# Performance work log

Measured on AMD Instinct MI355X. Metric: run time of the kernel, lower is better.

## Reference

```python
import jax, jax.numpy as jnp
import numpy as np

N = 8192
D = 256
LN_EPS = 1e-5
NORM_EPS = 1e-12


def _layernorm(h, gamma, beta):
    mu = jnp.mean(h, axis=-1, keepdims=True)
    var = jnp.var(h, axis=-1, keepdims=True)
    return (h - mu) * jax.lax.rsqrt(var + LN_EPS) * gamma + beta


def _elu(z):
    return jnp.where(z > 0, z, jnp.expm1(z))


def setup_inputs() -> dict:
    key = jax.random.key(0)
    ks = jax.random.split(key, 5)
    s = 1.0 / np.sqrt(D)  # torch Linear default-ish init scale
    h = jax.random.normal(ks[0], (N, D), dtype=jnp.float32)
    x = jax.random.normal(ks[1], (N, D), dtype=jnp.float32)
    Wk = jax.random.normal(ks[2], (D, D), dtype=jnp.float32) * s
    Wq = jax.random.normal(ks[3], (D, D), dtype=jnp.float32) * s
    Wv = jax.random.normal(ks[4], (D, D), dtype=jnp.float32) * s
    ln_gamma = jnp.ones((D,), dtype=jnp.float32)
    ln_beta = jnp.zeros((D,), dtype=jnp.float32)
    semantic_weight = -1.0
    mixing = jnp.array([[semantic_weight, semantic_weight], [0.0, 0.0]], dtype=jnp.float32)
    return {"h": h, "x": x, "Wk": Wk, "Wq": Wq, "Wv": Wv,
            "ln_gamma": ln_gamma, "ln_beta": ln_beta, "mixing": mixing}


def reference(h, x, Wk, Wq, Wv, ln_gamma, ln_beta, mixing):
    h0, x0 = h, x
    hn = _layernorm(h, ln_gamma, ln_beta)                      # [N, D]
    k = hn @ Wk                                                # [N, H]
    q = hn @ Wq                                                # [N, H]
    # semantic attention: softmax over rows of k q^T / sqrt(H)
    a_h = jax.nn.softmax((k @ q.T) * (D ** -0.5), axis=-1)     # [N, N]
    # structural attention: row-L2-normalized gram matrix of x
    g = x @ x.T                                                # [N, N]
    gnorm = jnp.linalg.norm(g, axis=-1, keepdims=True)
    a_x = g / jnp.maximum(gnorm, NORM_EPS)
    # learned 2x2 mixing, softmax over dim 0 (stack @ mixing.softmax(0))
    m = jax.nn.softmax(mixing, axis=0)
    a_h_mix = a_h * m[0, 0] + a_x * m[1, 0]
    a_x_mix = a_h * m[0, 1] + a_x * m[1, 1]
    h_new = _elu((a_h_mix @ hn) @ Wv)                          # [N, D]
    x_new = a_x_mix @ x                                        # [N, D]
    h_new = h_new + h0
    x_new = x_new + x0
    return (h_new, x_new)
```

## Files before the change

kernel.cpp:

```cpp
#include <hip/hip_runtime.h>

#define N 8192
#define D 256

typedef unsigned short u16;
typedef unsigned int u32;
typedef short bf16x8 __attribute__((ext_vector_type(8)));
typedef float f32x4 __attribute__((ext_vector_type(4)));

__device__ __forceinline__ u16 f2bf(float f) {
    u32 u = __float_as_uint(f);
    u += 0x7FFFu + ((u >> 16) & 1u);
    return (u16)(u >> 16);
}
__device__ __forceinline__ float bf2f(u16 v) {
    return __uint_as_float(((u32)v) << 16);
}

#define MFMA(a, b, c) __builtin_amdgcn_mfma_f32_16x16x32_bf16((a), (b), (c), 0, 0, 0)

__global__ __launch_bounds__(256) void k_prep_all(const float* __restrict__ h,
    const float* __restrict__ x, const float* __restrict__ gamma,
    const float* __restrict__ beta, u16* __restrict__ hnb, u16* __restrict__ xb,
    const float* __restrict__ Wk, const float* __restrict__ Wq,
    const float* __restrict__ Wv, u16* __restrict__ wkT,
    u16* __restrict__ wqT, u16* __restrict__ wvT)
{
    int bid = blockIdx.x;
    if (bid < 2048) {
        int lane = threadIdx.x & 63;
        int row = bid * 4 + (threadIdx.x >> 6);
        const float4 hv = ((const float4*)(h + (size_t)row * D))[lane];
        float s = hv.x + hv.y + hv.z + hv.w;
        float s2 = hv.x * hv.x + hv.y * hv.y + hv.z * hv.z + hv.w * hv.w;
#pragma unroll
        for (int m = 1; m < 64; m <<= 1) { s += __shfl_xor(s, m); s2 += __shfl_xor(s2, m); }
        float mu = s * (1.0f / D);
        float var = s2 * (1.0f / D) - mu * mu;
        float rstd = rsqrtf(var + 1e-5f);
        const float4 gv = ((const float4*)gamma)[lane];
        const float4 bv = ((const float4*)beta)[lane];
        ushort4 o;
        o.x = f2bf((hv.x - mu) * rstd * gv.x + bv.x);
        o.y = f2bf((hv.y - mu) * rstd * gv.y + bv.y);
        o.z = f2bf((hv.z - mu) * rstd * gv.z + bv.z);
        o.w = f2bf((hv.w - mu) * rstd * gv.w + bv.w);
        ((ushort4*)(hnb + (size_t)row * D))[lane] = o;
        const float4 xv = ((const float4*)(x + (size_t)row * D))[lane];
        ushort4 xo;
        xo.x = f2bf(xv.x); xo.y = f2bf(xv.y); xo.z = f2bf(xv.z); xo.w = f2bf(xv.w);
        ((ushort4*)(xb + (size_t)row * D))[lane] = xo;
    } else {
        int wid = bid - 2048;
        int sel = wid >> 8;
        int c = wid & 255;
        const float* src = sel == 0 ? Wk : (sel == 1 ? Wq : Wv);
        u16* dst = sel == 0 ? wkT : (sel == 1 ? wqT : wvT);
        int r = threadIdx.x;
        dst[c * D + r] = f2bf(src[r * D + c]);
    }
}

__global__ __launch_bounds__(256, 4) void k_trans_proj(const u16* __restrict__ hnb,
    u16* __restrict__ hnT, const u16* __restrict__ xb, u16* __restrict__ xT,
    const u16* __restrict__ wkT, const u16* __restrict__ wqT,
    u16* __restrict__ kb, u16* __restrict__ qb)
{
    __shared__ u16 tile[64][72];
    int bid = blockIdx.x;
    if (bid < 1024) {
        const u16* src = (bid >> 9) ? xb : hnb;
        u16* dst = (bid >> 9) ? xT : hnT;
        int xx = bid & 511;
        int jb = (xx & 127) * 64;
        int cb = (xx >> 7) * 64;
        int t = threadIdx.x;
#pragma unroll
        for (int i = 0; i < 2; ++i) {
            int id = t + i * 256;
            int r = id >> 3, ch = id & 7;
            uint4 v = *(const uint4*)(src + (size_t)(jb + r) * D + cb + ch * 8);
            *(uint4*)(&tile[r][ch * 8]) = v;
        }
        __syncthreads();
#pragma unroll
        for (int i = 0; i < 2; ++i) {
            int id = t + i * 256;
            int c = id >> 3, rch = id & 7;
            u16 vals[8] __attribute__((aligned(16)));
#pragma unroll
            for (int e = 0; e < 8; ++e) vals[e] = tile[rch * 8 + e][c];
            *(uint4*)(dst + (size_t)(cb + c) * N + jb + rch * 8) = *(const uint4*)vals;
        }
    } else {
        int pb = bid - 1024;
        int w = threadIdx.x >> 6;
        int lane = threadIdx.x & 63;
        int l16 = lane & 15, lhi = lane >> 4;
        int rows = pb * 16;
        const u16* BT = (w >> 1) ? wqT : wkT;
        u16* out = (w >> 1) ? qb : kb;
        int colbase = (w & 1) * 128;
        const f32x4 z4 = {0.f, 0.f, 0.f, 0.f};
        f32x4 acc[8] = {z4, z4, z4, z4, z4, z4, z4, z4};
#pragma unroll
        for (int ks = 0; ks < 8; ++ks) {
            bf16x8 a = *(const bf16x8*)(hnb + (size_t)(rows + l16) * D + ks * 32 + lhi * 8);
#pragma unroll
            for (int cf = 0; cf < 8; ++cf) {
                bf16x8 b = *(const bf16x8*)(BT + (size_t)(colbase + cf * 16 + l16) * D + ks * 32 + lhi * 8);
                acc[cf] = MFMA(a, b, acc[cf]);
            }
        }
#pragma unroll
        for (int cf = 0; cf < 8; ++cf)
#pragma unroll
            for (int jj = 0; jj < 4; ++jj)
                out[(size_t)(rows + lhi * 4 + jj) * D + colbase + cf * 16 + l16] = f2bf(acc[cf][jj]);
    }
}

__global__ __launch_bounds__(256) void k_small_nt(const u16* __restrict__ hnT,
    const u16* __restrict__ xT, float* __restrict__ part)
{
    const u16* P = blockIdx.y ? hnT : xT;
    const u16* Q = xT;
    int w = threadIdx.x >> 6;
    int lane = threadIdx.x & 63;
    int l16 = lane & 15, lhi = lane >> 4;
    int arow = blockIdx.x * 64;
    int bcol = w * 64;
    int n0b = blockIdx.z * 256;
    const f32x4 z4 = {0.f, 0.f, 0.f, 0.f};
    f32x4 acc[4][4];
#pragma unroll
    for (int ap = 0; ap < 4; ++ap)
#pragma unroll
        for (int cf = 0; cf < 4; ++cf) acc[ap][cf] = z4;
    for (int n0 = n0b; n0 < n0b + 256; n0 += 32) {
        bf16x8 b[4], a[4];
#pragma unroll
        for (int cf = 0; cf < 4; ++cf)
            b[cf] = *(const bf16x8*)(Q + (size_t)(bcol + cf * 16 + l16) * N + n0 + lhi * 8);
#pragma unroll
        for (int ap = 0; ap < 4; ++ap)
            a[ap] = *(const bf16x8*)(P + (size_t)(arow + ap * 16 + l16) * N + n0 + lhi * 8);
#pragma unroll
        for (int ap = 0; ap < 4; ++ap)
#pragma unroll
            for (int cf = 0; cf < 4; ++cf)
                acc[ap][cf] = MFMA(a[ap], b[cf], acc[ap][cf]);
    }
    float* dst = part + ((size_t)blockIdx.z * 2 + blockIdx.y) * 65536;
#pragma unroll
    for (int ap = 0; ap < 4; ++ap)
#pragma unroll
        for (int cf = 0; cf < 4; ++cf)
#pragma unroll
            for (int jj = 0; jj < 4; ++jj)
                dst[(size_t)(arow + ap * 16 + lhi * 4 + jj) * D + bcol + cf * 16 + l16] = acc[ap][cf][jj];
}

__global__ __launch_bounds__(256) void k_cast(const float* __restrict__ part,
    u16* __restrict__ Mb, u16* __restrict__ XHT)
{
    int t = blockIdx.x * 256 + threadIdx.x;
    int side = t >> 16, idx = t & 65535;
    float s = 0.f;
#pragma unroll
    for (int ks = 0; ks < 32; ++ks) s += part[((size_t)ks * 2 + side) * 65536 + idx];
    (side ? XHT : Mb)[idx] = f2bf(s);
}

__global__ __launch_bounds__(256, 4) void k_gemm16_dual(const u16* __restrict__ A,
    const u16* __restrict__ BT0, const u16* __restrict__ BT1,
    u16* __restrict__ out0, u16* __restrict__ out1)
{
    const u16* BT = blockIdx.y ? BT1 : BT0;
    u16* outb = blockIdx.y ? out1 : out0;
    int w = threadIdx.x >> 6;
    int lane = threadIdx.x & 63;
    int l16 = lane & 15, lhi = lane >> 4;
    int rows = blockIdx.x * 16;
    int cols = w * 64;
    const f32x4 z4 = {0.f, 0.f, 0.f, 0.f};
    f32x4 acc[4] = {z4, z4, z4, z4};
#pragma unroll
    for (int ks = 0; ks < 8; ++ks) {
        bf16x8 a = *(const bf16x8*)(A + (size_t)(rows + l16) * D + ks * 32 + lhi * 8);
#pragma unroll
        for (int cf = 0; cf < 4; ++cf) {
            bf16x8 b = *(const bf16x8*)(BT + (size_t)(cols + cf * 16 + l16) * D + ks * 32 + lhi * 8);
            acc[cf] = MFMA(a, b, acc[cf]);
        }
    }
#pragma unroll
    for (int cf = 0; cf < 4; ++cf)
#pragma unroll
        for (int jj = 0; jj < 4; ++jj)
            outb[(size_t)(rows + lhi * 4 + jj) * D + cols + cf * 16 + l16] = f2bf(acc[cf][jj]);
}

__global__ __launch_bounds__(256, 4) void k_gemm16_elu(const u16* __restrict__ A,
    const u16* __restrict__ BT, const float* __restrict__ res, float* __restrict__ outf)
{
    int w = threadIdx.x >> 6;
    int lane = threadIdx.x & 63;
    int l16 = lane & 15, lhi = lane >> 4;
    int rows = blockIdx.x * 16;
    int cols = w * 64;
    const f32x4 z4 = {0.f, 0.f, 0.f, 0.f};
    f32x4 acc[4] = {z4, z4, z4, z4};
#pragma unroll
    for (int ks = 0; ks < 8; ++ks) {
        bf16x8 a = *(const bf16x8*)(A + (size_t)(rows + l16) * D + ks * 32 + lhi * 8);
#pragma unroll
        for (int cf = 0; cf < 4; ++cf) {
            bf16x8 b = *(const bf16x8*)(BT + (size_t)(cols + cf * 16 + l16) * D + ks * 32 + lhi * 8);
            acc[cf] = MFMA(a, b, acc[cf]);
        }
    }
#pragma unroll
    for (int cf = 0; cf < 4; ++cf)
#pragma unroll
        for (int jj = 0; jj < 4; ++jj) {
            int r = rows + lhi * 4 + jj;
            int c = cols + cf * 16 + l16;
            float v = acc[cf][jj];
            float z = v > 0.f ? v : expm1f(v);
            outf[(size_t)r * D + c] = z + res[(size_t)r * D + c];
        }
}

__global__ __launch_bounds__(512, 4) void k_fused(const u16* __restrict__ kb,
    const u16* __restrict__ qb, const u16* __restrict__ hnT,
    const u16* __restrict__ xT, u16* __restrict__ accP, float* __restrict__ lpart)
{
    __shared__ u16 AK[64 * 256];
    __shared__ u16 P[64 * 256];
    const int tid = threadIdx.x;
    const int w = tid >> 6;
    const int lane = tid & 63;
    const int l16 = lane & 15, lhi = lane >> 4;
    const int wgid = blockIdx.x;
    const int xcd = wgid & 7;
    const int js = xcd >> 1;
    const int rb = ((wgid >> 3) << 1) | (xcd & 1);
    const int R0 = rb * 64;
    const int jbase = js * 2048;

    {
        int r = tid >> 3, sb = (tid & 7) * 4;
        const u16* src = kb + (size_t)(R0 + r) * D + sb * 8;
#pragma unroll
        for (int i = 0; i < 4; ++i) {
            bf16x8 v = *(const bf16x8*)(src + i * 8);
            int s = sb + i;
            int slotp = (s & 16) | ((s & 15) ^ (r & 15));
            *(bf16x8*)(AK + r * 256 + slotp * 8) = v;
        }
    }
    __syncthreads();

    const int rg = w & 1;
    const int jf = w >> 1;
    const int t2 = w >> 2;
    const int ch = w & 3;
    const u16* T = t2 ? xT : hnT;
    const u16* Tb0 = T + (size_t)(ch * 64 + 0 * 16 + l16) * N + lhi * 8;
    const u16* Tb1 = T + (size_t)(ch * 64 + 1 * 16 + l16) * N + lhi * 8;
    const u16* Tb2 = T + (size_t)(ch * 64 + 2 * 16 + l16) * N + lhi * 8;
    const u16* Tb3 = T + (size_t)(ch * 64 + 3 * 16 + l16) * N + lhi * 8;

    const f32x4 z4 = {0.f, 0.f, 0.f, 0.f};
    f32x4 acc[16];
#pragma unroll
    for (int i = 0; i < 16; ++i) acc[i] = z4;
    f32x4 red2[2] = {z4, z4};
    bf16x8 tp0[4], tp1[4];

    for (int it = 0; it < 8; ++it) {
        const int jb = jbase + it * 256;
        asm volatile("s_waitcnt lgkmcnt(0)\n\ts_barrier" ::: "memory");

#pragma unroll
        for (int s = 0; s < 2; ++s) {
            const int jc = jb + s * 128 + jf * 32;
            f32x4 cs00 = z4, cs01 = z4, cs10 = z4, cs11 = z4;
#pragma unroll
            for (int ks = 0; ks < 8; ++ks) {
                int r0 = rg * 32 + l16;
                int r1 = r0 + 16;
                int sq = ks * 4 + lhi;
                int slx = (sq & 16) | ((sq & 15) ^ l16);
                bf16x8 a0 = *(const bf16x8*)(AK + r0 * 256 + slx * 8);
                bf16x8 a1 = *(const bf16x8*)(AK + r1 * 256 + slx * 8);
                const u16* Bq = qb + (size_t)(jc + l16) * D + ks * 32 + lhi * 8;
                bf16x8 b0 = *(const bf16x8*)(Bq);
                bf16x8 b1 = *(const bf16x8*)(Bq + 16 * D);
                cs00 = MFMA(a0, b0, cs00);
                cs01 = MFMA(a0, b1, cs01);
                cs10 = MFMA(a1, b0, cs10);
                cs11 = MFMA(a1, b1, cs11);
            }
#pragma unroll
            for (int rf = 0; rf < 2; ++rf)
#pragma unroll
                for (int cfr = 0; cfr < 2; ++cfr) {
                    f32x4 s4 = rf ? (cfr ? cs11 : cs10) : (cfr ? cs01 : cs00);
#pragma unroll
                    for (int jj = 0; jj < 4; ++jj) {
                        int row = rg * 32 + rf * 16 + lhi * 4 + jj;
                        int col = s * 128 + jf * 32 + cfr * 16 + l16;
                        float pv = __expf(s4[jj] * 0.0625f);
                        red2[rf][jj] += pv;
                        int slot = (col >> 3) ^ (row & 15);
                        *(u16*)((char*)P + row * 512 + slot * 16 + (col & 7) * 2) = f2bf(pv);
                    }
                }
        }
        tp0[0] = *(const bf16x8*)(Tb0 + jb); tp0[1] = *(const bf16x8*)(Tb1 + jb);
        tp0[2] = *(const bf16x8*)(Tb2 + jb); tp0[3] = *(const bf16x8*)(Tb3 + jb);
        tp1[0] = *(const bf16x8*)(Tb0 + jb + 32); tp1[1] = *(const bf16x8*)(Tb1 + jb + 32);
        tp1[2] = *(const bf16x8*)(Tb2 + jb + 32); tp1[3] = *(const bf16x8*)(Tb3 + jb + 32);
        asm volatile("s_waitcnt lgkmcnt(0)\n\ts_barrier" ::: "memory");

        __builtin_amdgcn_s_setprio(1);
        const char* Pb = (const char*)P;
#define PV_STEP(KF, TP)                                                             \
        {                                                                           \
            bf16x8 pa0 = *(const bf16x8*)(Pb + (0 * 16 + l16) * 512 + ((((KF) * 4 + lhi) ^ l16) << 4)); \
            bf16x8 pa1 = *(const bf16x8*)(Pb + (1 * 16 + l16) * 512 + ((((KF) * 4 + lhi) ^ l16) << 4)); \
            bf16x8 pa2 = *(const bf16x8*)(Pb + (2 * 16 + l16) * 512 + ((((KF) * 4 + lhi) ^ l16) << 4)); \
            bf16x8 pa3 = *(const bf16x8*)(Pb + (3 * 16 + l16) * 512 + ((((KF) * 4 + lhi) ^ l16) << 4)); \
            acc[0]  = MFMA(pa0, TP[0], acc[0]);  acc[1]  = MFMA(pa0, TP[1], acc[1]);  \
            acc[2]  = MFMA(pa0, TP[2], acc[2]);  acc[3]  = MFMA(pa0, TP[3], acc[3]);  \
            acc[4]  = MFMA(pa1, TP[0], acc[4]);  acc[5]  = MFMA(pa1, TP[1], acc[5]);  \
            acc[6]  = MFMA(pa1, TP[2], acc[6]);  acc[7]  = MFMA(pa1, TP[3], acc[7]);  \
            acc[8]  = MFMA(pa2, TP[0], acc[8]);  acc[9]  = MFMA(pa2, TP[1], acc[9]);  \
            acc[10] = MFMA(pa2, TP[2], acc[10]); acc[11] = MFMA(pa2, TP[3], acc[11]); \
            acc[12] = MFMA(pa3, TP[0], acc[12]); acc[13] = MFMA(pa3, TP[1], acc[13]); \
            acc[14] = MFMA(pa3, TP[2], acc[14]); acc[15] = MFMA(pa3, TP[3], acc[15]); \
            if ((KF) + 2 < 8) {                                                     \
                TP[0] = *(const bf16x8*)(Tb0 + jb + ((KF) + 2) * 32);               \
                TP[1] = *(const bf16x8*)(Tb1 + jb + ((KF) + 2) * 32);               \
                TP[2] = *(const bf16x8*)(Tb2 + jb + ((KF) + 2) * 32);               \
                TP[3] = *(const bf16x8*)(Tb3 + jb + ((KF) + 2) * 32);               \
            }                                                                       \
        }
        PV_STEP(0, tp0)
        PV_STEP(1, tp1)
        PV_STEP(2, tp0)
        PV_STEP(3, tp1)
        PV_STEP(4, tp0)
        PV_STEP(5, tp1)
        PV_STEP(6, tp0)
        PV_STEP(7, tp1)
#undef PV_STEP
        __builtin_amdgcn_s_setprio(0);
    }

    {
        u16* base = accP + ((((size_t)js * 128 + rb) * 8 + w) * 64) * 64 + lane;
#pragma unroll
        for (int rf = 0; rf < 4; ++rf)
#pragma unroll
            for (int cf = 0; cf < 4; ++cf)
#pragma unroll
                for (int jj = 0; jj < 4; ++jj) {
                    int v = (rf * 4 + cf) * 4 + jj;
                    __builtin_nontemporal_store(f2bf(acc[rf * 4 + cf][jj]), base + (size_t)v * 64);
                }
    }
#pragma unroll
    for (int rf = 0; rf < 2; ++rf)
#pragma unroll
        for (int m = 1; m < 16; m <<= 1) {
            red2[rf][0] += __shfl_xor(red2[rf][0], m);
            red2[rf][1] += __shfl_xor(red2[rf][1], m);
            red2[rf][2] += __shfl_xor(red2[rf][2], m);
            red2[rf][3] += __shfl_xor(red2[rf][3], m);
        }
    if (l16 == 0)
#pragma unroll
        for (int rf = 0; rf < 2; ++rf)
#pragma unroll
            for (int jj = 0; jj < 4; ++jj)
                atomicAdd(lpart + R0 + rg * 32 + rf * 16 + lhi * 4 + jj, red2[rf][jj]);
}

__global__ __launch_bounds__(256) void k_combine(const u16* __restrict__ accP,
    const float* __restrict__ lpart, const u16* __restrict__ Uh,
    const u16* __restrict__ Ux, const u16* __restrict__ xb,
    const float* __restrict__ mixing, const float* __restrict__ x0,
    u16* __restrict__ hmixb, float* __restrict__ outx)
{
    __shared__ float sred[2][2];
    int t = threadIdx.x;
    int rl = t >> 7;
    int q = t & 127;
    int r = blockIdx.x * 2 + rl;

    float sg;
    {
        int idx = q * 2;
        const u16* up = Ux + (size_t)r * D + idx;
        const u16* xp = xb + (size_t)r * D + idx;
        float part = bf2f(up[0]) * bf2f(xp[0]) + bf2f(up[1]) * bf2f(xp[1]);
#pragma unroll
        for (int m = 1; m < 64; m <<= 1) part += __shfl_xor(part, m);
        int wv = q >> 6;
        if ((t & 63) == 0) sred[rl][wv] = part;
        __syncthreads();
        sg = sred[rl][0] + sred[rl][1];
    }
    float inv_l = 1.0f / lpart[r];
    float inv_g = 1.0f / fmaxf(sqrtf(fmaxf(sg, 0.f)), 1e-12f);
    float e00 = __expf(mixing[0]), e10 = __expf(mixing[2]);
    float c00 = e00 / (e00 + e10), c10 = e10 / (e00 + e10);
    float e01 = __expf(mixing[1]), e11 = __expf(mixing[3]);
    float c01 = e01 / (e01 + e11), c11 = e11 / (e01 + e11);
    float stx = c00 * inv_l, sty = c10 * inv_g;
    float stz = c01 * inv_l, stw = c11 * inv_g;

    int rb = r >> 6, rr = r & 63;
    int t2 = q >> 6;
    int cc = (q & 63) * 4;
    int wv2 = t2 * 4 + (cc >> 6);
    int rf = rr >> 4, lhi = (rr >> 2) & 3, jj = rr & 3;
    int cf = (cc >> 4) & 3, l16 = cc & 15;
    int v = (rf * 4 + cf) * 4 + jj;
    int lane = lhi * 16 + l16;
    float v0 = 0.f, v1 = 0.f, v2 = 0.f, v3 = 0.f;
#pragma unroll
    for (int s = 0; s < 4; ++s) {
        const u16* bp = accP + ((((size_t)s * 128 + rb) * 8 + wv2) * 64 + v) * 64 + lane;
        ushort4 a = *(const ushort4*)bp;
        v0 += bf2f(a.x); v1 += bf2f(a.y); v2 += bf2f(a.z); v3 += bf2f(a.w);
    }
    if (t2 == 0) {
        int c = cc;
        ushort4 u = *(const ushort4*)(Uh + (size_t)r * D + c);
        ushort4 o;
        o.x = f2bf(stx * v0 + sty * bf2f(u.x));
        o.y = f2bf(stx * v1 + sty * bf2f(u.y));
        o.z = f2bf(stx * v2 + sty * bf2f(u.z));
        o.w = f2bf(stx * v3 + sty * bf2f(u.w));
        *(ushort4*)(hmixb + (size_t)r * D + c) = o;
    } else {
        int c = cc;
        ushort4 u = *(const ushort4*)(Ux + (size_t)r * D + c);
        float4 xv = *(const float4*)(x0 + (size_t)r * D + c);
        float4 o;
        o.x = stz * v0 + stw * bf2f(u.x) + xv.x;
        o.y = stz * v1 + stw * bf2f(u.y) + xv.y;
        o.z = stz * v2 + stw * bf2f(u.z) + xv.z;
        o.w = stz * v3 + stw * bf2f(u.w) + xv.w;
        *(float4*)(outx + (size_t)r * D + c) = o;
    }
}

extern "C" void kernel_launch(void* const* d_in, const int* in_sizes, int n_in,
                              void* d_out, int out_size, void* d_ws, size_t ws_size,
                              hipStream_t stream)
{
    const float* h = (const float*)d_in[0];
    const float* x = (const float*)d_in[1];
    const float* Wk = (const float*)d_in[2];
    const float* Wq = (const float*)d_in[3];
    const float* Wv = (const float*)d_in[4];
    const float* gamma = (const float*)d_in[5];
    const float* beta = (const float*)d_in[6];
    const float* mixing = (const float*)d_in[7];

    char* p = (char*)d_ws;
    const size_t ND2 = (size_t)N * D * 2;
    u16* hnb = (u16*)p; p += ND2;
    u16* xb = (u16*)p; p += ND2;
    u16* kb = (u16*)p; p += ND2;
    u16* qb = (u16*)p; p += ND2;
    u16* hnT = (u16*)p; p += ND2;
    u16* xT = (u16*)p; p += ND2;
    u16* Ux = (u16*)p; p += ND2;
    u16* wkT = (u16*)p; p += (size_t)D * D * 2;
    u16* wqT = (u16*)p; p += (size_t)D * D * 2;
    u16* wvT = (u16*)p; p += (size_t)D * D * 2;
    u16* Mb = (u16*)p; p += (size_t)D * D * 2;
    u16* XHT = (u16*)p; p += (size_t)D * D * 2;
    u16* accP = (u16*)p; p += (size_t)4 * N * 512 * 2;
    float* ntpart = (float*)accP;
    float* lpart = (float*)p; p += (size_t)N * 4;
    u16* Uh = hnb;
    u16* hmixb = kb;

    float* outh = (float*)d_out;
    float* outx = outh + (size_t)N * D;

    hipMemsetAsync(lpart, 0, (size_t)N * 4, stream);
    k_prep_all<<<2048 + 768, 256, 0, stream>>>(h, x, gamma, beta, hnb, xb,
                                               Wk, Wq, Wv, wkT, wqT, wvT);
    k_trans_proj<<<1024 + 512, 256, 0, stream>>>(hnb, hnT, xb, xT, wkT, wqT, kb, qb);
    k_small_nt<<<dim3(4, 2, 32), 256, 0, stream>>>(hnT, xT, ntpart);
    k_cast<<<512, 256, 0, stream>>>(ntpart, Mb, XHT);
    k_gemm16_dual<<<dim3(512, 2), 256, 0, stream>>>(xb, Mb, XHT, Ux, Uh);
    k_fused<<<512, 512, 0, stream>>>(kb, qb, hnT, xT, accP, lpart);
    k_combine<<<N / 2, 256, 0, stream>>>(accP, lpart, Uh, Ux, xb, mixing, x, hmixb, outx);
    k_gemm16_elu<<<512, 256, 0, stream>>>(hmixb, wvT, h, outh);
}
```

Measured before the change: 367.6 us.

## Halve fused attention row tile to 32 and prefetch Q fragments across iterations

```diff
diff --git a/kernel.cpp b/kernel.cpp
--- a/kernel.cpp
+++ b/kernel.cpp
@@ -236,8 +236,8 @@
     const u16* __restrict__ qb, const u16* __restrict__ hnT,
     const u16* __restrict__ xT, u16* __restrict__ accP, float* __restrict__ lpart)
 {
-    __shared__ u16 AK[64 * 256];
-    __shared__ u16 P[64 * 256];
+    __shared__ u16 AK[32 * 256];
+    __shared__ u16 P[32 * 256];
     const int tid = threadIdx.x;
     const int w = tid >> 6;
     const int lane = tid & 63;
@@ -246,24 +246,22 @@
     const int xcd = wgid & 7;
     const int js = xcd >> 1;
     const int rb = ((wgid >> 3) << 1) | (xcd & 1);
-    const int R0 = rb * 64;
+    const int R0 = rb * 32;
     const int jbase = js * 2048;
 
     {
-        int r = tid >> 3, sb = (tid & 7) * 4;
+        int r = tid >> 4, sb = (tid & 15) * 2;
         const u16* src = kb + (size_t)(R0 + r) * D + sb * 8;
 #pragma unroll
-        for (int i = 0; i < 4; ++i) {
+        for (int i = 0; i < 2; ++i) {
             bf16x8 v = *(const bf16x8*)(src + i * 8);
             int s = sb + i;
             int slotp = (s & 16) | ((s & 15) ^ (r & 15));
             *(bf16x8*)(AK + r * 256 + slotp * 8) = v;
         }
     }
-    __syncthreads();
-
-    const int rg = w & 1;
-    const int jf = w >> 1;
+
+    const int jf = w;
     const int t2 = w >> 2;
     const int ch = w & 3;
     const u16* T = t2 ? xT : hnT;
@@ -273,49 +271,52 @@
     const u16* Tb3 = T + (size_t)(ch * 64 + 3 * 16 + l16) * N + lhi * 8;
 
     const f32x4 z4 = {0.f, 0.f, 0.f, 0.f};
-    f32x4 acc[16];
-#pragma unroll
-    for (int i = 0; i < 16; ++i) acc[i] = z4;
+    f32x4 acc[8];
+#pragma unroll
+    for (int i = 0; i < 8; ++i) acc[i] = z4;
     f32x4 red2[2] = {z4, z4};
-    bf16x8 tp0[4], tp1[4];
+    bf16x8 tp0[4], tp1[4], qpre[8];
+
+    __syncthreads();
+
+#pragma unroll
+    for (int ks = 0; ks < 8; ++ks)
+        qpre[ks] = *(const bf16x8*)(qb + (size_t)(jbase + jf * 32 + l16) * D + ks * 32 + lhi * 8);
 
     for (int it = 0; it < 8; ++it) {
         const int jb = jbase + it * 256;
         asm volatile("s_waitcnt lgkmcnt(0)\n\ts_barrier" ::: "memory");
 
-#pragma unroll
-        for (int s = 0; s < 2; ++s) {
-            const int jc = jb + s * 128 + jf * 32;
-            f32x4 cs00 = z4, cs01 = z4, cs10 = z4, cs11 = z4;
+        {
+            const int jc = jb + jf * 32;
+            f32x4 cs0 = z4, cs1 = z4, cs2 = z4, cs3 = z4;
 #pragma unroll
             for (int ks = 0; ks < 8; ++ks) {
-                int r0 = rg * 32 + l16;
-                int r1 = r0 + 16;
                 int sq = ks * 4 + lhi;
                 int slx = (sq & 16) | ((sq & 15) ^ l16);
-                bf16x8 a0 = *(const bf16x8*)(AK + r0 * 256 + slx * 8);
-                bf16x8 a1 = *(const bf16x8*)(AK + r1 * 256 + slx * 8);
-                const u16* Bq = qb + (size_t)(jc + l16) * D + ks * 32 + lhi * 8;
-                bf16x8 b0 = *(const bf16x8*)(Bq);
-                bf16x8 b1 = *(const bf16x8*)(Bq + 16 * D);
-                cs00 = MFMA(a0, b0, cs00);
-                cs01 = MFMA(a0, b1, cs01);
-                cs10 = MFMA(a1, b0, cs10);
-                cs11 = MFMA(a1, b1, cs11);
+                bf16x8 a0 = *(const bf16x8*)(AK + l16 * 256 + slx * 8);
+                bf16x8 a1 = *(const bf16x8*)(AK + (16 + l16) * 256 + slx * 8);
+                bf16x8 b0 = qpre[ks];
+                bf16x8 b1 = *(const bf16x8*)(qb + (size_t)(jc + 16 + l16) * D + ks * 32 + lhi * 8);
+                cs0 = MFMA(a0, b0, cs0);
+                cs1 = MFMA(a0, b1, cs1);
+                cs2 = MFMA(a1, b0, cs2);
+                cs3 = MFMA(a1, b1, cs3);
             }
 #pragma unroll
             for (int rf = 0; rf < 2; ++rf)
 #pragma unroll
                 for (int cfr = 0; cfr < 2; ++cfr) {
-                    f32x4 s4 = rf ? (cfr ? cs11 : cs10) : (cfr ? cs01 : cs00);
+                    f32x4 s4 = rf ? (cfr ? cs3 : cs2) : (cfr ? cs1 : cs0);
 #pragma unroll
                     for (int jj = 0; jj < 4; ++jj) {
-                        int row = rg * 32 + rf * 16 + lhi * 4 + jj;
-                        int col = s * 128 + jf * 32 + cfr * 16 + l16;
+                        int row = rf * 16 + lhi * 4 + jj;
+                        int col = jf * 32 + cfr * 16 + l16;
                         float pv = __expf(s4[jj] * 0.0625f);
                         red2[rf][jj] += pv;
-                        int slot = (col >> 3) ^ (row & 15);
-                        *(u16*)((char*)P + row * 512 + slot * 16 + (col & 7) * 2) = f2bf(pv);
+                        int s5 = col >> 3;
+                        int slotp = (s5 & 16) | ((s5 & 15) ^ (row & 15));
+                        *(u16*)((char*)P + row * 512 + slotp * 16 + (col & 7) * 2) = f2bf(pv);
                     }
                 }
         }
@@ -325,22 +326,25 @@
         tp1[2] = *(const bf16x8*)(Tb2 + jb + 32); tp1[3] = *(const bf16x8*)(Tb3 + jb + 32);
         asm volatile("s_waitcnt lgkmcnt(0)\n\ts_barrier" ::: "memory");
 
+        {
+            const int jn = jbase + ((it + 1) & 7) * 256 + jf * 32;
+#pragma unroll
+            for (int ks = 0; ks < 8; ++ks)
+                qpre[ks] = *(const bf16x8*)(qb + (size_t)(jn + l16) * D + ks * 32 + lhi * 8);
+        }
+
         __builtin_amdgcn_s_setprio(1);
         const char* Pb = (const char*)P;
 #define PV_STEP(KF, TP)                                                             \
         {                                                                           \
-            bf16x8 pa0 = *(const bf16x8*)(Pb + (0 * 16 + l16) * 512 + ((((KF) * 4 + lhi) ^ l16) << 4)); \
-            bf16x8 pa1 = *(const bf16x8*)(Pb + (1 * 16 + l16) * 512 + ((((KF) * 4 + lhi) ^ l16) << 4)); \
-            bf16x8 pa2 = *(const bf16x8*)(Pb + (2 * 16 + l16) * 512 + ((((KF) * 4 + lhi) ^ l16) << 4)); \
-            bf16x8 pa3 = *(const bf16x8*)(Pb + (3 * 16 + l16) * 512 + ((((KF) * 4 + lhi) ^ l16) << 4)); \
-            acc[0]  = MFMA(pa0, TP[0], acc[0]);  acc[1]  = MFMA(pa0, TP[1], acc[1]);  \
-            acc[2]  = MFMA(pa0, TP[2], acc[2]);  acc[3]  = MFMA(pa0, TP[3], acc[3]);  \
-            acc[4]  = MFMA(pa1, TP[0], acc[4]);  acc[5]  = MFMA(pa1, TP[1], acc[5]);  \
-            acc[6]  = MFMA(pa1, TP[2], acc[6]);  acc[7]  = MFMA(pa1, TP[3], acc[7]);  \
-            acc[8]  = MFMA(pa2, TP[0], acc[8]);  acc[9]  = MFMA(pa2, TP[1], acc[9]);  \
-            acc[10] = MFMA(pa2, TP[2], acc[10]); acc[11] = MFMA(pa2, TP[3], acc[11]); \
-            acc[12] = MFMA(pa3, TP[0], acc[12]); acc[13] = MFMA(pa3, TP[1], acc[13]); \
-            acc[14] = MFMA(pa3, TP[2], acc[14]); acc[15] = MFMA(pa3, TP[3], acc[15]); \
+            int sq_ = (KF) * 4 + lhi;                                               \
+            int slx_ = (sq_ & 16) | ((sq_ & 15) ^ l16);                             \
+            bf16x8 pa0 = *(const bf16x8*)(Pb + l16 * 512 + slx_ * 16);              \
+            bf16x8 pa1 = *(const bf16x8*)(Pb + (16 + l16) * 512 + slx_ * 16);       \
+            acc[0] = MFMA(pa0, TP[0], acc[0]);  acc[1] = MFMA(pa0, TP[1], acc[1]);  \
+            acc[2] = MFMA(pa0, TP[2], acc[2]);  acc[3] = MFMA(pa0, TP[3], acc[3]);  \
+            acc[4] = MFMA(pa1, TP[0], acc[4]);  acc[5] = MFMA(pa1, TP[1], acc[5]);  \
+            acc[6] = MFMA(pa1, TP[2], acc[6]);  acc[7] = MFMA(pa1, TP[3], acc[7]);  \
             if ((KF) + 2 < 8) {                                                     \
                 TP[0] = *(const bf16x8*)(Tb0 + jb + ((KF) + 2) * 32);               \
                 TP[1] = *(const bf16x8*)(Tb1 + jb + ((KF) + 2) * 32);               \
@@ -361,9 +365,9 @@
     }
 
     {
-        u16* base = accP + ((((size_t)js * 128 + rb) * 8 + w) * 64) * 64 + lane;
-#pragma unroll
-        for (int rf = 0; rf < 4; ++rf)
+        u16* base = accP + ((((size_t)js * 256 + rb) * 8 + w) * 32) * 64 + lane;
+#pragma unroll
+        for (int rf = 0; rf < 2; ++rf)
 #pragma unroll
             for (int cf = 0; cf < 4; ++cf)
 #pragma unroll
@@ -386,7 +390,7 @@
         for (int rf = 0; rf < 2; ++rf)
 #pragma unroll
             for (int jj = 0; jj < 4; ++jj)
-                atomicAdd(lpart + R0 + rg * 32 + rf * 16 + lhi * 4 + jj, red2[rf][jj]);
+                atomicAdd(lpart + R0 + rf * 16 + lhi * 4 + jj, red2[rf][jj]);
 }
 
 __global__ __launch_bounds__(256) void k_combine(const u16* __restrict__ accP,
@@ -423,7 +427,7 @@
     float stx = c00 * inv_l, sty = c10 * inv_g;
     float stz = c01 * inv_l, stw = c11 * inv_g;
 
-    int rb = r >> 6, rr = r & 63;
+    int rb = r >> 5, rr = r & 31;
     int t2 = q >> 6;
     int cc = (q & 63) * 4;
     int wv2 = t2 * 4 + (cc >> 6);
@@ -434,7 +438,7 @@
     float v0 = 0.f, v1 = 0.f, v2 = 0.f, v3 = 0.f;
 #pragma unroll
     for (int s = 0; s < 4; ++s) {
-        const u16* bp = accP + ((((size_t)s * 128 + rb) * 8 + wv2) * 64 + v) * 64 + lane;
+        const u16* bp = accP + ((((size_t)s * 256 + rb) * 8 + wv2) * 32 + v) * 64 + lane;
         ushort4 a = *(const ushort4*)bp;
         v0 += bf2f(a.x); v1 += bf2f(a.y); v2 += bf2f(a.z); v3 += bf2f(a.w);
     }
@@ -503,7 +507,7 @@
     k_small_nt<<<dim3(4, 2, 32), 256, 0, stream>>>(hnT, xT, ntpart);
     k_cast<<<512, 256, 0, stream>>>(ntpart, Mb, XHT);
     k_gemm16_dual<<<dim3(512, 2), 256, 0, stream>>>(xb, Mb, XHT, Ux, Uh);
-    k_fused<<<512, 512, 0, stream>>>(kb, qb, hnT, xT, accP, lpart);
+    k_fused<<<1024, 512, 0, stream>>>(kb, qb, hnT, xT, accP, lpart);
     k_combine<<<N / 2, 256, 0, stream>>>(accP, lpart, Uh, Ux, xb, mixing, x, hmixb, outx);
     k_gemm16_elu<<<512, 256, 0, stream>>>(hmixb, wvT, h, outh);
 }
```

New measurement: 498.5 us. 1.36x slower.

## Split fused attention blocks by value target and prefetch Q fragments

Applied to the files above, without the earlier changes.

```diff
diff --git a/kernel.cpp b/kernel.cpp
--- a/kernel.cpp
+++ b/kernel.cpp
@@ -245,7 +245,9 @@
     const int wgid = blockIdx.x;
     const int xcd = wgid & 7;
     const int js = xcd >> 1;
-    const int rb = ((wgid >> 3) << 1) | (xcd & 1);
+    const int idx = ((wgid >> 3) << 1) | (xcd & 1);
+    const int rb = idx >> 1;
+    const int t2 = idx & 1;
     const int R0 = rb * 64;
     const int jbase = js * 2048;
 
@@ -260,24 +262,24 @@
             *(bf16x8*)(AK + r * 256 + slotp * 8) = v;
         }
     }
-    __syncthreads();
 
     const int rg = w & 1;
     const int jf = w >> 1;
-    const int t2 = w >> 2;
-    const int ch = w & 3;
+    const int ch = w;
     const u16* T = t2 ? xT : hnT;
-    const u16* Tb0 = T + (size_t)(ch * 64 + 0 * 16 + l16) * N + lhi * 8;
-    const u16* Tb1 = T + (size_t)(ch * 64 + 1 * 16 + l16) * N + lhi * 8;
-    const u16* Tb2 = T + (size_t)(ch * 64 + 2 * 16 + l16) * N + lhi * 8;
-    const u16* Tb3 = T + (size_t)(ch * 64 + 3 * 16 + l16) * N + lhi * 8;
+    const u16* Tb0 = T + (size_t)(ch * 32 + 0 * 16 + l16) * N + lhi * 8;
+    const u16* Tb1 = T + (size_t)(ch * 32 + 1 * 16 + l16) * N + lhi * 8;
 
     const f32x4 z4 = {0.f, 0.f, 0.f, 0.f};
-    f32x4 acc[16];
-#pragma unroll
-    for (int i = 0; i < 16; ++i) acc[i] = z4;
+    f32x4 acc[8];
+#pragma unroll
+    for (int i = 0; i < 8; ++i) acc[i] = z4;
     f32x4 red2[2] = {z4, z4};
-    bf16x8 tp0[4], tp1[4];
+    bf16x8 tp0[2], tp1[2], qpre[8];
+
+#pragma unroll
+    for (int ks = 0; ks < 8; ++ks)
+        qpre[ks] = *(const bf16x8*)(qb + (size_t)(jbase + jf * 32 + l16) * D + ks * 32 + lhi * 8);
 
     for (int it = 0; it < 8; ++it) {
         const int jb = jbase + it * 256;
@@ -296,7 +298,7 @@
                 bf16x8 a0 = *(const bf16x8*)(AK + r0 * 256 + slx * 8);
                 bf16x8 a1 = *(const bf16x8*)(AK + r1 * 256 + slx * 8);
                 const u16* Bq = qb + (size_t)(jc + l16) * D + ks * 32 + lhi * 8;
-                bf16x8 b0 = *(const bf16x8*)(Bq);
+                bf16x8 b0 = (s == 0) ? qpre[ks] : *(const bf16x8*)(Bq);
                 bf16x8 b1 = *(const bf16x8*)(Bq + 16 * D);
                 cs00 = MFMA(a0, b0, cs00);
                 cs01 = MFMA(a0, b1, cs01);
@@ -319,33 +321,33 @@
                     }
                 }
         }
-        tp0[0] = *(const bf16x8*)(Tb0 + jb); tp0[1] = *(const bf16x8*)(Tb1 + jb);
-        tp0[2] = *(const bf16x8*)(Tb2 + jb); tp0[3] = *(const bf16x8*)(Tb3 + jb);
+        tp0[0] = *(const bf16x8*)(Tb0 + jb);      tp0[1] = *(const bf16x8*)(Tb1 + jb);
         tp1[0] = *(const bf16x8*)(Tb0 + jb + 32); tp1[1] = *(const bf16x8*)(Tb1 + jb + 32);
-        tp1[2] = *(const bf16x8*)(Tb2 + jb + 32); tp1[3] = *(const bf16x8*)(Tb3 + jb + 32);
         asm volatile("s_waitcnt lgkmcnt(0)\n\ts_barrier" ::: "memory");
+
+        {
+            const int jn = jbase + ((it + 1) & 7) * 256 + jf * 32;
+#pragma unroll
+            for (int ks = 0; ks < 8; ++ks)
+                qpre[ks] = *(const bf16x8*)(qb + (size_t)(jn + l16) * D + ks * 32 + lhi * 8);
+        }
 
         __builtin_amdgcn_s_setprio(1);
         const char* Pb = (const char*)P;
 #define PV_STEP(KF, TP)                                                             \
         {                                                                           \
-            bf16x8 pa0 = *(const bf16x8*)(Pb + (0 * 16 + l16) * 512 + ((((KF) * 4 + lhi) ^ l16) << 4)); \
-            bf16x8 pa1 = *(const bf16x8*)(Pb + (1 * 16 + l16) * 512 + ((((KF) * 4 + lhi) ^ l16) << 4)); \
-            bf16x8 pa2 = *(const bf16x8*)(Pb + (2 * 16 + l16) * 512 + ((((KF) * 4 + lhi) ^ l16) << 4)); \
-            bf16x8 pa3 = *(const bf16x8*)(Pb + (3 * 16 + l16) * 512 + ((((KF) * 4 + lhi) ^ l16) << 4)); \
-            acc[0]  = MFMA(pa0, TP[0], acc[0]);  acc[1]  = MFMA(pa0, TP[1], acc[1]);  \
-            acc[2]  = MFMA(pa0, TP[2], acc[2]);  acc[3]  = MFMA(pa0, TP[3], acc[3]);  \
-            acc[4]  = MFMA(pa1, TP[0], acc[4]);  acc[5]  = MFMA(pa1, TP[1], acc[5]);  \
-            acc[6]  = MFMA(pa1, TP[2], acc[6]);  acc[7]  = MFMA(pa1, TP[3], acc[7]);  \
-            acc[8]  = MFMA(pa2, TP[0], acc[8]);  acc[9]  = MFMA(pa2, TP[1], acc[9]);  \
-            acc[10] = MFMA(pa2, TP[2], acc[10]); acc[11] = MFMA(pa2, TP[3], acc[11]); \
-            acc[12] = MFMA(pa3, TP[0], acc[12]); acc[13] = MFMA(pa3, TP[1], acc[13]); \
-            acc[14] = MFMA(pa3, TP[2], acc[14]); acc[15] = MFMA(pa3, TP[3], acc[15]); \
+            int off_ = ((((KF) * 4 + lhi) ^ l16) << 4);                             \
+            bf16x8 pa0 = *(const bf16x8*)(Pb + (0 * 16 + l16) * 512 + off_);        \
+            bf16x8 pa1 = *(const bf16x8*)(Pb + (1 * 16 + l16) * 512 + off_);        \
+            bf16x8 pa2 = *(const bf16x8*)(Pb + (2 * 16 + l16) * 512 + off_);        \
+            bf16x8 pa3 = *(const bf16x8*)(Pb + (3 * 16 + l16) * 512 + off_);        \
+            acc[0] = MFMA(pa0, TP[0], acc[0]);  acc[1] = MFMA(pa0, TP[1], acc[1]);  \
+            acc[2] = MFMA(pa1, TP[0], acc[2]);  acc[3] = MFMA(pa1, TP[1], acc[3]);  \
+            acc[4] = MFMA(pa2, TP[0], acc[4]);  acc[5] = MFMA(pa2, TP[1], acc[5]);  \
+            acc[6] = MFMA(pa3, TP[0], acc[6]);  acc[7] = MFMA(pa3, TP[1], acc[7]);  \
             if ((KF) + 2 < 8) {                                                     \
                 TP[0] = *(const bf16x8*)(Tb0 + jb + ((KF) + 2) * 32);               \
                 TP[1] = *(const bf16x8*)(Tb1 + jb + ((KF) + 2) * 32);               \
-                TP[2] = *(const bf16x8*)(Tb2 + jb + ((KF) + 2) * 32);               \
-                TP[3] = *(const bf16x8*)(Tb3 + jb + ((KF) + 2) * 32);               \
             }                                                                       \
         }
         PV_STEP(0, tp0)
@@ -361,32 +363,34 @@
     }
 
     {
-        u16* base = accP + ((((size_t)js * 128 + rb) * 8 + w) * 64) * 64 + lane;
+        u16* base = accP + ((((size_t)js * 128 + rb) * 16 + t2 * 8 + w) * 32) * 64 + lane;
 #pragma unroll
         for (int rf = 0; rf < 4; ++rf)
 #pragma unroll
-            for (int cf = 0; cf < 4; ++cf)
+            for (int cf = 0; cf < 2; ++cf)
 #pragma unroll
                 for (int jj = 0; jj < 4; ++jj) {
-                    int v = (rf * 4 + cf) * 4 + jj;
-                    __builtin_nontemporal_store(f2bf(acc[rf * 4 + cf][jj]), base + (size_t)v * 64);
+                    int v = (rf * 2 + cf) * 4 + jj;
+                    __builtin_nontemporal_store(f2bf(acc[rf * 2 + cf][jj]), base + (size_t)v * 64);
                 }
     }
-#pragma unroll
-    for (int rf = 0; rf < 2; ++rf)
-#pragma unroll
-        for (int m = 1; m < 16; m <<= 1) {
-            red2[rf][0] += __shfl_xor(red2[rf][0], m);
-            red2[rf][1] += __shfl_xor(red2[rf][1], m);
-            red2[rf][2] += __shfl_xor(red2[rf][2], m);
-            red2[rf][3] += __shfl_xor(red2[rf][3], m);
-        }
-    if (l16 == 0)
+    if (t2 == 0) {
 #pragma unroll
         for (int rf = 0; rf < 2; ++rf)
 #pragma unroll
-            for (int jj = 0; jj < 4; ++jj)
-                atomicAdd(lpart + R0 + rg * 32 + rf * 16 + lhi * 4 + jj, red2[rf][jj]);
+            for (int m = 1; m < 16; m <<= 1) {
+                red2[rf][0] += __shfl_xor(red2[rf][0], m);
+                red2[rf][1] += __shfl_xor(red2[rf][1], m);
+                red2[rf][2] += __shfl_xor(red2[rf][2], m);
+                red2[rf][3] += __shfl_xor(red2[rf][3], m);
+            }
+        if (l16 == 0)
+#pragma unroll
+            for (int rf = 0; rf < 2; ++rf)
+#pragma unroll
+                for (int jj = 0; jj < 4; ++jj)
+                    atomicAdd(lpart + R0 + rg * 32 + rf * 16 + lhi * 4 + jj, red2[rf][jj]);
+    }
 }
 
 __global__ __launch_bounds__(256) void k_combine(const u16* __restrict__ accP,
@@ -426,15 +430,15 @@
     int rb = r >> 6, rr = r & 63;
     int t2 = q >> 6;
     int cc = (q & 63) * 4;
-    int wv2 = t2 * 4 + (cc >> 6);
+    int wv2 = t2 * 8 + (cc >> 5);
     int rf = rr >> 4, lhi = (rr >> 2) & 3, jj = rr & 3;
-    int cf = (cc >> 4) & 3, l16 = cc & 15;
-    int v = (rf * 4 + cf) * 4 + jj;
+    int cf = (cc >> 4) & 1, l16 = cc & 15;
+    int v = (rf * 2 + cf) * 4 + jj;
     int lane = lhi * 16 + l16;
     float v0 = 0.f, v1 = 0.f, v2 = 0.f, v3 = 0.f;
 #pragma unroll
     for (int s = 0; s < 4; ++s) {
-        const u16* bp = accP + ((((size_t)s * 128 + rb) * 8 + wv2) * 64 + v) * 64 + lane;
+        const u16* bp = accP + ((((size_t)s * 128 + rb) * 16 + wv2) * 32 + v) * 64 + lane;
         ushort4 a = *(const ushort4*)bp;
         v0 += bf2f(a.x); v1 += bf2f(a.y); v2 += bf2f(a.z); v3 += bf2f(a.w);
     }
@@ -503,7 +507,7 @@
     k_small_nt<<<dim3(4, 2, 32), 256, 0, stream>>>(hnT, xT, ntpart);
     k_cast<<<512, 256, 0, stream>>>(ntpart, Mb, XHT);
     k_gemm16_dual<<<dim3(512, 2), 256, 0, stream>>>(xb, Mb, XHT, Ux, Uh);
-    k_fused<<<512, 512, 0, stream>>>(kb, qb, hnT, xT, accP, lpart);
+    k_fused<<<1024, 512, 0, stream>>>(kb, qb, hnT, xT, accP, lpart);
     k_combine<<<N / 2, 256, 0, stream>>>(accP, lpart, Uh, Ux, xb, mixing, x, hmixb, outx);
     k_gemm16_elu<<<512, 256, 0, stream>>>(hmixb, wvT, h, outh);
 }
```

Measured after the change: 473.1 us. 1.29x slower.
